# Performance work log

Measured on AMD Instinct MI355X. Metric: run time of the kernel, lower is better.

Reference implementation:

```python
import jax, jax.numpy as jnp
import numpy as np

B, P, D = 64, 128, 128   # clouds, points per cloud, vec_dim
N = B * P                # 8192 nodes
EPS = 1e-5


def _complete_graph_edges():
    # knn_graph with k == total node count => complete graph per cloud (no self loops)
    i = np.arange(P)
    ii, jj = np.meshgrid(i, i, indexing='ij')
    m = ii != jj
    li, lj = ii[m], jj[m]                      # [P*(P-1)] local pairs
    off = (np.arange(B) * P)[:, None]          # cloud offsets
    src = (off + li[None, :]).reshape(-1)      # neighbor index
    dst = (off + lj[None, :]).reshape(-1)      # center index
    return jnp.asarray(src, jnp.int32), jnp.asarray(dst, jnp.int32)


def setup_inputs() -> dict:
    key = jax.random.key(0)
    ks = jax.random.split(key, 4)
    src, dst = _complete_graph_edges()
    return {
        'x': jax.random.normal(ks[0], (N, D), jnp.float32),
        'xyz': jax.random.normal(ks[1], (N, 3), jnp.float32),
        'W_xyz': jax.random.normal(ks[2], (3, D), jnp.float32) * 0.1,
        'bn_gamma': jnp.ones((D,), jnp.float32),
        'bn_beta': jnp.zeros((D,), jnp.float32),
        'W1': jax.random.normal(ks[3], (D, D), jnp.float32) * 0.05,
        'b1': jnp.zeros((D,), jnp.float32),
        'ln_gamma': jnp.ones((D,), jnp.float32),
        'ln_beta': jnp.zeros((D,), jnp.float32),
        'src': src,
        'dst': dst,
    }


def reference(x, xyz, W_xyz, bn_gamma, bn_beta, W1, b1, ln_gamma, ln_beta, src, dst):
    n = x.shape[0]
    rela_xyz = xyz[src] - xyz[dst]                         # [E, 3]
    rela_x = x[src] - x[dst]                               # [E, D]
    dist = jnp.sqrt(jnp.sum(rela_xyz * rela_xyz, axis=-1))  # [E]
    w = jnp.exp(-dist)[:, None]                            # [E, 1]

    # weighted linear + relu, pool by src (global_add_pool over node index)
    h1 = jax.nn.relu((w * rela_x) @ W1 + b1)               # [E, D]
    p1 = jax.ops.segment_sum(h1, src, num_segments=n)      # [N, D]
    mu = jnp.mean(p1, axis=-1, keepdims=True)
    var = jnp.var(p1, axis=-1, keepdims=True)
    x = x + ((p1 - mu) / jnp.sqrt(var + EPS)) * ln_gamma + ln_beta

    # xyz projection branch, BatchNorm1d (training-mode batch stats)
    h2 = jax.nn.relu(rela_xyz @ W_xyz)                     # [E, D]
    p2 = jax.ops.segment_sum(h2, src, num_segments=n)      # [N, D]
    bmu = jnp.mean(p2, axis=0)
    bvar = jnp.var(p2, axis=0)
    x = x + ((p2 - bmu) / jnp.sqrt(bvar + EPS)) * bn_gamma + bn_beta
    return x
```

## Files before the change

### kernel.cpp

```cpp
#include <hip/hip_runtime.h>
#include <stdint.h>

#define EPS 1e-5f
#define N_NODES 8192

typedef __attribute__((ext_vector_type(8))) short short8;
typedef __attribute__((ext_vector_type(4))) float floatx4;
typedef __attribute__((ext_vector_type(2))) float floatx2;
typedef __attribute__((ext_vector_type(4))) unsigned short ushortx4;

__device__ __forceinline__ unsigned short f2bf(float f) {
    uint32_t u = __float_as_uint(f);
    u += 0x7FFFu + ((u >> 16) & 1u);
    return (unsigned short)(u >> 16);
}

__global__ __launch_bounds__(256) void prep_kernel(
    const float* __restrict__ x, const float* __restrict__ W1,
    unsigned short* __restrict__ xb, unsigned short* __restrict__ w1t,
    float* __restrict__ stat_ws)
{
    const int bx = blockIdx.x, tid = threadIdx.x;
    if (bx < 1024) {
        const int base = bx * 1024 + tid * 4;
        floatx4 v = *(const floatx4*)(x + base);
        ushortx4 o = { f2bf(v[0]), f2bf(v[1]), f2bf(v[2]), f2bf(v[3]) };
        *(ushortx4*)(xb + base) = o;
    } else {
        const int b2 = bx - 1024;
        const int n = b2 * 8 + (tid >> 5);
        const int k = (tid & 31) * 4;
#pragma unroll
        for (int e = 0; e < 4; ++e)
            w1t[n * 128 + k + e] = f2bf(W1[(k + e) * 128 + n]);
        if (b2 == 0) {
            floatx4 z = {0.f, 0.f, 0.f, 0.f};
            *(floatx4*)(stat_ws + tid * 4) = z;
        }
    }
}

__global__ __launch_bounds__(64) void gemm_y_kernel(
    const unsigned short* __restrict__ xb, const unsigned short* __restrict__ w1t,
    float* __restrict__ y)
{
    const int lane = threadIdx.x;
    const int ml = lane & 15, q = lane >> 4;
    const int rb = blockIdx.x * 16;

    short8 afrag[4];
#pragma unroll
    for (int c = 0; c < 4; ++c)
        afrag[c] = *(const short8*)(xb + (rb + ml) * 128 + c * 32 + q * 8);

#pragma unroll
    for (int nt = 0; nt < 8; ++nt) {
        floatx4 acc = {0.f, 0.f, 0.f, 0.f};
        const int ncol = nt * 16 + ml;
#pragma unroll
        for (int c = 0; c < 4; ++c) {
            short8 b = *(const short8*)(w1t + ncol * 128 + c * 32 + q * 8);
            acc = __builtin_amdgcn_mfma_f32_16x16x32_bf16(afrag[c], b, acc, 0, 0, 0);
        }
#pragma unroll
        for (int r = 0; r < 4; ++r)
            y[(rb + q * 4 + r) * 128 + ncol] = acc[r];
    }
}

__global__ __launch_bounds__(256, 4) void cloud_main_kernel(
    const float* __restrict__ x, const float* __restrict__ xyz,
    const float* __restrict__ W_xyz, const float* __restrict__ b1,
    const float* __restrict__ ln_gamma, const float* __restrict__ ln_beta,
    const float* __restrict__ y_ws, float* __restrict__ p2_ws,
    float* __restrict__ stat_ws, float* __restrict__ out)
{
    __shared__ float smem[1616];
    float* s_w   = smem;
    float* s_xyz = smem + 1024;
    float* s_p1  = smem;
    float* s_bn  = smem + 1088;
    float* s_mu  = smem + 1600;
    float* s_rs  = smem + 1608;

    const int bx = blockIdx.x;
    const int c = bx & 63, s = bx >> 6;
    const int tid = threadIdx.x;
    const int d = tid & 127, g = tid >> 7;
    const int node0 = c * 128;
    const int i0 = s * 8;
    const int iL0 = i0 + g * 4;

    if (tid < 128) {
        const float* p = xyz + (node0 + tid) * 3;
        s_xyz[tid * 4 + 0] = p[0];
        s_xyz[tid * 4 + 1] = p[1];
        s_xyz[tid * 4 + 2] = p[2];
        s_xyz[tid * 4 + 3] = 0.f;
    }
    __syncthreads();

    for (int e = tid; e < 1024; e += 256) {
        const int j = e >> 3, ii = e & 7, ia = i0 + ii;
        float dx = s_xyz[ia * 4]     - s_xyz[j * 4];
        float dy = s_xyz[ia * 4 + 1] - s_xyz[j * 4 + 1];
        float dz = s_xyz[ia * 4 + 2] - s_xyz[j * 4 + 2];
        s_w[j * 8 + ii] = __expf(-sqrtf(dx * dx + dy * dy + dz * dz));
    }
    __syncthreads();

    const float w0 = W_xyz[d], w1c = W_xyz[128 + d], w2c = W_xyz[256 + d];
    const float b1d = b1[d];

    floatx2 yi[2], zi[2], a1[2], a2[2];
#pragma unroll
    for (int r = 0; r < 4; ++r) {
        const int ia = iL0 + r;
        yi[r >> 1][r & 1] = y_ws[(node0 + ia) * 128 + d];
        zi[r >> 1][r & 1] = s_xyz[ia * 4] * w0 + s_xyz[ia * 4 + 1] * w1c
                          + s_xyz[ia * 4 + 2] * w2c;
        a1[r >> 1][r & 1] = 0.f;
        a2[r >> 1][r & 1] = 0.f;
    }
    const floatx2 b1v = {b1d, b1d};
    const floatx2 zv2 = {0.f, 0.f};
    const float* yrow = y_ws + node0 * 128 + d;

#pragma unroll 4
    for (int j = 0; j < 128; ++j) {
        const float yj = yrow[j * 128];
        floatx4 xj = *(const floatx4*)(s_xyz + j * 4);
        const float zj = xj[0] * w0 + xj[1] * w1c + xj[2] * w2c;
        floatx4 wv = *(const floatx4*)(s_w + j * 8 + g * 4);
        floatx2 wlo = {wv[0], wv[1]}, whi = {wv[2], wv[3]};
        floatx2 yj2 = {yj, yj}, zj2 = {zj, zj};
        floatx2 t0 = wlo * (yi[0] - yj2) + b1v;
        floatx2 t1 = whi * (yi[1] - yj2) + b1v;
        a1[0] += __builtin_elementwise_max(t0, zv2);
        a1[1] += __builtin_elementwise_max(t1, zv2);
        a2[0] += __builtin_elementwise_max(zi[0] - zj2, zv2);
        a2[1] += __builtin_elementwise_max(zi[1] - zj2, zv2);
    }
    {
        const float sc = fmaxf(b1d, 0.f);
        floatx2 scv = {sc, sc};
        a1[0] -= scv; a1[1] -= scv;
    }
    __syncthreads();

    {
        float bs = 0.f, bq = 0.f;
#pragma unroll
        for (int r = 0; r < 4; ++r) {
            s_p1[(g * 4 + r) * 136 + d] = a1[r >> 1][r & 1];
            float v2 = a2[r >> 1][r & 1];
            bs += v2;
            bq += v2 * v2;
        }
        s_bn[g * 256 + d] = bs;
        s_bn[g * 256 + 128 + d] = bq;
    }
    __syncthreads();

    {
        const int ii = tid >> 5, sub = tid & 31;
        floatx4 v = *(const floatx4*)(s_p1 + ii * 136 + sub * 4);
        float ps = v[0] + v[1] + v[2] + v[3];
        float pq = v[0] * v[0] + v[1] * v[1] + v[2] * v[2] + v[3] * v[3];
#pragma unroll
        for (int m = 1; m < 32; m <<= 1) {
            ps += __shfl_xor(ps, m, 64);
            pq += __shfl_xor(pq, m, 64);
        }
        if (sub == 0) {
            float mu = ps * (1.f / 128.f);
            float var = pq * (1.f / 128.f) - mu * mu;
            s_mu[ii] = mu;
            s_rs[ii] = rsqrtf(var + EPS);
        }
    }
    if (tid < 128) {
        const int bank = (s & 3) * 256;
        atomicAdd(stat_ws + bank + d,       s_bn[d] + s_bn[256 + d]);
        atomicAdd(stat_ws + bank + 128 + d, s_bn[128 + d] + s_bn[384 + d]);
    }
    __syncthreads();

    const float lng = ln_gamma[d], lnb = ln_beta[d];
#pragma unroll
    for (int r = 0; r < 4; ++r) {
        const int ii = g * 4 + r;
        const int gi = node0 + iL0 + r;
        float o = x[gi * 128 + d] + (a1[r >> 1][r & 1] - s_mu[ii]) * s_rs[ii] * lng + lnb;
        out[gi * 128 + d] = o;
        p2_ws[gi * 128 + d] = a2[r >> 1][r & 1];
    }
}

__global__ __launch_bounds__(256) void finalize_kernel(
    const float* __restrict__ p2_ws, const float* __restrict__ stat_ws,
    const float* __restrict__ bn_gamma, const float* __restrict__ bn_beta,
    float* __restrict__ out)
{
    __shared__ float sA[128], sB[128];
    const int tid = threadIdx.x;
    if (tid < 128) {
        float sm = 0.f, sq = 0.f;
#pragma unroll
        for (int b = 0; b < 4; ++b) {
            sm += stat_ws[b * 256 + tid];
            sq += stat_ws[b * 256 + 128 + tid];
        }
        float mu = sm * (1.f / 8192.f);
        float var = sq * (1.f / 8192.f) - mu * mu;
        float rs = rsqrtf(var + EPS);
        float A = rs * bn_gamma[tid];
        sA[tid] = A;
        sB[tid] = bn_beta[tid] - mu * A;
    }
    __syncthreads();
    const int base = (blockIdx.x * 256 + tid) * 4;
    const int d0 = base & 127;
    floatx4 p2 = *(const floatx4*)(p2_ws + base);
    floatx4 o  = *(const floatx4*)(out + base);
#pragma unroll
    for (int e = 0; e < 4; ++e)
        o[e] += p2[e] * sA[d0 + e] + sB[d0 + e];
    *(floatx4*)(out + base) = o;
}

extern "C" void kernel_launch(void* const* d_in, const int* in_sizes, int n_in,
                              void* d_out, int out_size, void* d_ws, size_t ws_size,
                              hipStream_t stream) {
    const float* x        = (const float*)d_in[0];
    const float* xyz      = (const float*)d_in[1];
    const float* W_xyz    = (const float*)d_in[2];
    const float* bn_gamma = (const float*)d_in[3];
    const float* bn_beta  = (const float*)d_in[4];
    const float* W1       = (const float*)d_in[5];
    const float* b1       = (const float*)d_in[6];
    const float* ln_gamma = (const float*)d_in[7];
    const float* ln_beta  = (const float*)d_in[8];
    float* out = (float*)d_out;

    float* y_ws    = (float*)d_ws;
    float* p2_ws   = y_ws + N_NODES * 128;
    float* stat_ws = p2_ws + N_NODES * 128;
    unsigned short* xb  = (unsigned short*)(stat_ws + 1024);
    unsigned short* w1t = xb + N_NODES * 128;

    prep_kernel<<<1040, 256, 0, stream>>>(x, W1, xb, w1t, stat_ws);
    gemm_y_kernel<<<512, 64, 0, stream>>>(xb, w1t, y_ws);
    cloud_main_kernel<<<1024, 256, 0, stream>>>(x, xyz, W_xyz, b1, ln_gamma, ln_beta,
                                                y_ws, p2_ws, stat_ws, out);
    finalize_kernel<<<1024, 256, 0, stream>>>(p2_ws, stat_ws, bn_gamma, bn_beta, out);
}
```

Baseline: 118.3 us.

## Split neighbor loop across thread halves instead of splitting centers

Each thread now handles all 8 center rows but only half of the 128 neighbors, so every y_ws neighbor row and xyz load feeds 8 accumulations instead of 4, halving global y reads per thread. The two halves' partial sums are combined through a new shared-memory reduction buffer before the LayerNorm and BatchNorm statistics. In exchange, register use roughly doubles for accumulators and inputs, which can lower occupancy under the 256x4 launch bounds. Only half the threads do the epilogue, and shared memory grows.

```diff
diff --git a/kernel.cpp b/kernel.cpp
--- a/kernel.cpp
+++ b/kernel.cpp
@@ -75,21 +75,20 @@
     const float* __restrict__ y_ws, float* __restrict__ p2_ws,
     float* __restrict__ stat_ws, float* __restrict__ out)
 {
-    __shared__ float smem[1616];
-    float* s_w   = smem;
-    float* s_xyz = smem + 1024;
-    float* s_p1  = smem;
-    float* s_bn  = smem + 1088;
-    float* s_mu  = smem + 1600;
-    float* s_rs  = smem + 1608;
+    __shared__ float s_xyz[512];
+    __shared__ float s_w[1024];
+    __shared__ float s_red[2048];
+    __shared__ float s_p1[1088];
+    __shared__ float s_bn[256];
+    __shared__ float s_mu[8];
+    __shared__ float s_rs[8];
 
     const int bx = blockIdx.x;
     const int c = bx & 63, s = bx >> 6;
     const int tid = threadIdx.x;
-    const int d = tid & 127, g = tid >> 7;
+    const int d = tid & 127, h = tid >> 7;
     const int node0 = c * 128;
     const int i0 = s * 8;
-    const int iL0 = i0 + g * 4;
 
     if (tid < 128) {
         const float* p = xyz + (node0 + tid) * 3;
@@ -111,54 +110,69 @@
 
     const float w0 = W_xyz[d], w1c = W_xyz[128 + d], w2c = W_xyz[256 + d];
     const float b1d = b1[d];
-
-    floatx2 yi[2], zi[2], a1[2], a2[2];
-#pragma unroll
-    for (int r = 0; r < 4; ++r) {
-        const int ia = iL0 + r;
+    const floatx2 b1v = {b1d, b1d};
+    const floatx2 zv2 = {0.f, 0.f};
+
+    floatx2 yi[4], zi[4], a1[4], a2[4];
+#pragma unroll
+    for (int r = 0; r < 8; ++r) {
+        const int ia = i0 + r;
         yi[r >> 1][r & 1] = y_ws[(node0 + ia) * 128 + d];
         zi[r >> 1][r & 1] = s_xyz[ia * 4] * w0 + s_xyz[ia * 4 + 1] * w1c
                           + s_xyz[ia * 4 + 2] * w2c;
         a1[r >> 1][r & 1] = 0.f;
         a2[r >> 1][r & 1] = 0.f;
     }
-    const floatx2 b1v = {b1d, b1d};
-    const floatx2 zv2 = {0.f, 0.f};
-    const float* yrow = y_ws + node0 * 128 + d;
+
+    const float* yrow = y_ws + (node0 + h * 64) * 128 + d;
+    const float* wp = s_w + h * 64 * 8;
+    const float* xp = s_xyz + h * 64 * 4;
 
 #pragma unroll 4
-    for (int j = 0; j < 128; ++j) {
+    for (int j = 0; j < 64; ++j) {
         const float yj = yrow[j * 128];
-        floatx4 xj = *(const floatx4*)(s_xyz + j * 4);
+        floatx4 xj = *(const floatx4*)(xp + j * 4);
         const float zj = xj[0] * w0 + xj[1] * w1c + xj[2] * w2c;
-        floatx4 wv = *(const floatx4*)(s_w + j * 8 + g * 4);
-        floatx2 wlo = {wv[0], wv[1]}, whi = {wv[2], wv[3]};
-        floatx2 yj2 = {yj, yj}, zj2 = {zj, zj};
-        floatx2 t0 = wlo * (yi[0] - yj2) + b1v;
-        floatx2 t1 = whi * (yi[1] - yj2) + b1v;
-        a1[0] += __builtin_elementwise_max(t0, zv2);
-        a1[1] += __builtin_elementwise_max(t1, zv2);
+        floatx4 wa = *(const floatx4*)(wp + j * 8);
+        floatx4 wb = *(const floatx4*)(wp + j * 8 + 4);
+        const floatx2 yj2 = {yj, yj}, zj2 = {zj, zj};
+        floatx2 wlo = {wa[0], wa[1]}, wmd = {wa[2], wa[3]};
+        floatx2 wh0 = {wb[0], wb[1]}, wh1 = {wb[2], wb[3]};
+        a1[0] += __builtin_elementwise_max(wlo * (yi[0] - yj2) + b1v, zv2);
+        a1[1] += __builtin_elementwise_max(wmd * (yi[1] - yj2) + b1v, zv2);
+        a1[2] += __builtin_elementwise_max(wh0 * (yi[2] - yj2) + b1v, zv2);
+        a1[3] += __builtin_elementwise_max(wh1 * (yi[3] - yj2) + b1v, zv2);
         a2[0] += __builtin_elementwise_max(zi[0] - zj2, zv2);
         a2[1] += __builtin_elementwise_max(zi[1] - zj2, zv2);
-    }
-    {
-        const float sc = fmaxf(b1d, 0.f);
-        floatx2 scv = {sc, sc};
-        a1[0] -= scv; a1[1] -= scv;
-    }
-    __syncthreads();
-
-    {
+        a2[2] += __builtin_elementwise_max(zi[2] - zj2, zv2);
+        a2[3] += __builtin_elementwise_max(zi[3] - zj2, zv2);
+    }
+    __syncthreads();
+
+    if (h == 1) {
+#pragma unroll
+        for (int r = 0; r < 8; ++r) {
+            s_red[r * 128 + d]        = a1[r >> 1][r & 1];
+            s_red[1024 + r * 128 + d] = a2[r >> 1][r & 1];
+        }
+    }
+    __syncthreads();
+
+    if (h == 0) {
+        const float selfc = fmaxf(b1d, 0.f);
         float bs = 0.f, bq = 0.f;
 #pragma unroll
-        for (int r = 0; r < 4; ++r) {
-            s_p1[(g * 4 + r) * 136 + d] = a1[r >> 1][r & 1];
-            float v2 = a2[r >> 1][r & 1];
+        for (int r = 0; r < 8; ++r) {
+            float v1 = a1[r >> 1][r & 1] + s_red[r * 128 + d] - selfc;
+            float v2 = a2[r >> 1][r & 1] + s_red[1024 + r * 128 + d];
+            a1[r >> 1][r & 1] = v1;
+            a2[r >> 1][r & 1] = v2;
+            s_p1[r * 136 + d] = v1;
             bs += v2;
             bq += v2 * v2;
         }
-        s_bn[g * 256 + d] = bs;
-        s_bn[g * 256 + 128 + d] = bq;
+        s_bn[d] = bs;
+        s_bn[128 + d] = bq;
     }
     __syncthreads();
 
@@ -181,19 +195,20 @@
     }
     if (tid < 128) {
         const int bank = (s & 3) * 256;
-        atomicAdd(stat_ws + bank + d,       s_bn[d] + s_bn[256 + d]);
-        atomicAdd(stat_ws + bank + 128 + d, s_bn[128 + d] + s_bn[384 + d]);
-    }
-    __syncthreads();
-
-    const float lng = ln_gamma[d], lnb = ln_beta[d];
-#pragma unroll
-    for (int r = 0; r < 4; ++r) {
-        const int ii = g * 4 + r;
-        const int gi = node0 + iL0 + r;
-        float o = x[gi * 128 + d] + (a1[r >> 1][r & 1] - s_mu[ii]) * s_rs[ii] * lng + lnb;
-        out[gi * 128 + d] = o;
-        p2_ws[gi * 128 + d] = a2[r >> 1][r & 1];
+        atomicAdd(stat_ws + bank + d,       s_bn[d]);
+        atomicAdd(stat_ws + bank + 128 + d, s_bn[128 + d]);
+    }
+    __syncthreads();
+
+    if (h == 0) {
+        const float lng = ln_gamma[d], lnb = ln_beta[d];
+#pragma unroll
+        for (int r = 0; r < 8; ++r) {
+            const int gi = node0 + i0 + r;
+            float o = x[gi * 128 + d] + (a1[r >> 1][r & 1] - s_mu[r]) * s_rs[r] * lng + lnb;
+            out[gi * 128 + d] = o;
+            p2_ws[gi * 128 + d] = a2[r >> 1][r & 1];
+        }
     }
 }
 
```

After: 113.0 us. 4.4% less time.
